# Kernel tuning notes

Measured on AMD Instinct MI355X. Metric: run time of the kernel, lower is better.

## Reference

```python
import jax, jax.numpy as jnp
import numpy as np

N_EMBD = 1024
N_HEAD = 16
HEAD_SIZE = N_EMBD // N_HEAD
SEQ_LEN = 2048


def setup_inputs() -> dict:
    key = jax.random.key(0)
    k_x, k_wa, k_ba, k_wp, k_bp = jax.random.split(key, 5)
    s = 0.02
    return {
        "x": jax.random.normal(k_x, (4, SEQ_LEN, N_EMBD), dtype=jnp.float32),
        "w_attn": jax.random.normal(k_wa, (N_EMBD, 3 * N_EMBD), dtype=jnp.float32) * s,
        "b_attn": jax.random.normal(k_ba, (3 * N_EMBD,), dtype=jnp.float32) * s,
        "w_proj": jax.random.normal(k_wp, (N_EMBD, N_EMBD), dtype=jnp.float32) * s,
        "b_proj": jax.random.normal(k_bp, (N_EMBD,), dtype=jnp.float32) * s,
    }


def reference(x, w_attn, b_attn, w_proj, b_proj):
    B, T, C = x.shape
    H, D = N_HEAD, HEAD_SIZE
    qkv = x @ w_attn + b_attn                      # [B,T,3C]
    q, k, v = jnp.split(qkv, 3, axis=-1)
    q = q.reshape(B, T, H, D).transpose(0, 2, 1, 3)  # [B,H,T,D]
    k = k.reshape(B, T, H, D).transpose(0, 2, 1, 3)
    v = v.reshape(B, T, H, D).transpose(0, 2, 1, 3)
    att = jnp.einsum('bhqd,bhkd->bhqk', q, k) / jnp.sqrt(jnp.float32(D))
    causal = jnp.tril(jnp.ones((T, T), dtype=bool))
    att = jnp.where(causal[None, None], att, jnp.float32(-jnp.inf))
    att = jax.nn.softmax(att, axis=-1)
    out = jnp.einsum('bhqk,bhkd->bhqd', att, v)    # [B,H,T,D]
    out = out.transpose(0, 2, 1, 3).reshape(B, T, C)
    return out @ w_proj + b_proj
```

## Files before the change

kernel.cpp:

```cpp
#include <hip/hip_runtime.h>

typedef short short8 __attribute__((ext_vector_type(8)));
typedef short short4v __attribute__((ext_vector_type(4)));
typedef float f32x4 __attribute__((ext_vector_type(4)));
typedef unsigned uint2v __attribute__((ext_vector_type(2)));

__device__ __forceinline__ float bf2f(short b) {
  unsigned u = ((unsigned)(unsigned short)b) << 16;
  return __builtin_bit_cast(float, u);
}
__device__ __forceinline__ short f2bf(float f) {
  unsigned u = __builtin_bit_cast(unsigned, f);
  u += 0x7fffu + ((u >> 16) & 1u);
  return (short)(u >> 16);
}
__device__ __forceinline__ unsigned cvt_pk_bf16(float lo, float hi) {
  unsigned r;
  asm("v_cvt_pk_bf16_f32 %0, %1, %2" : "=v"(r) : "v"(lo), "v"(hi));
  return r;
}

__device__ __forceinline__ void gload_lds16(const void* g, void* l) {
  __builtin_amdgcn_global_load_lds(
      (const __attribute__((address_space(1))) unsigned int*)g,
      (__attribute__((address_space(3))) unsigned int*)l, 16, 0, 0);
}

__device__ __forceinline__ short8 lds_frag(const short* tile, int row, int kc, int l4) {
  int chunk = (kc * 4 + l4) ^ (row & 7);
  return *(const short8*)&tile[row * 64 + chunk * 8];
}

__global__ __launch_bounds__(256) void k_convert_bf16(const float* __restrict__ in,
                                                      short* __restrict__ out, int n8) {
  int i = blockIdx.x * 256 + threadIdx.x;
  if (i >= n8) return;
  const float4* p = (const float4*)in;
  float4 a = p[2 * i], b = p[2 * i + 1];
  short8 o;
  o[0] = f2bf(a.x); o[1] = f2bf(a.y); o[2] = f2bf(a.z); o[3] = f2bf(a.w);
  o[4] = f2bf(b.x); o[5] = f2bf(b.y); o[6] = f2bf(b.z); o[7] = f2bf(b.w);
  ((short8*)out)[i] = o;
}

__global__ __launch_bounds__(256) void k_transpose_w(const float* __restrict__ w,
                                                     short* __restrict__ wT, int K, int N) {
  __shared__ float t[32][33];
  int nt = N >> 5;
  int rt = blockIdx.x / nt, ct = blockIdx.x % nt;
  int tx = threadIdx.x & 31, ty = threadIdx.x >> 5;
#pragma unroll
  for (int i = 0; i < 4; ++i) {
    int r = ty * 4 + i;
    t[r][tx] = w[(size_t)(rt * 32 + r) * N + ct * 32 + tx];
  }
  __syncthreads();
#pragma unroll
  for (int i = 0; i < 4; ++i) {
    int r = ty * 4 + i;
    wT[(size_t)(ct * 32 + r) * K + rt * 32 + tx] = f2bf(t[tx][r]);
  }
}

template <bool BF16OUT>
__global__ __launch_bounds__(512, 1) void k_gemm8p(const short* __restrict__ A,
                                                   const short* __restrict__ Bt,
                                                   const float* __restrict__ bias,
                                                   void* __restrict__ Cout,
                                                   int M, int N, int K) {
  __shared__ __align__(16) short Ab[2][256 * 64];
  __shared__ __align__(16) short Bb[2][256 * 64];
  int nt = N >> 8;
  int nwg = gridDim.x;
  int bid = blockIdx.x;
  int swz = (bid & 7) * (nwg >> 3) + (bid >> 3);
  int mt = swz / nt, ct = swz % nt;
  int tid = threadIdx.x, w = tid >> 6, lane = tid & 63;
  int l15 = lane & 15, l4 = lane >> 4;
  int wm = w >> 2, wn = w & 3;
  const short* Abase = A + (size_t)mt * 256 * K;
  const short* Bbase = Bt + (size_t)ct * 256 * K;
  int NT = K >> 6;

  int srow = lane >> 3;
  int slc = (lane & 7) ^ srow;

  auto stage = [&](const short* gbase, short* dstTile, int kt, int half) {
#pragma unroll
    for (int i = 0; i < 2; ++i) {
      int rowg = half * 128 + i * 64 + w * 8;
      gload_lds16(gbase + (size_t)(rowg + srow) * K + kt * 64 + slc * 8,
                  dstTile + (size_t)rowg * 64);
    }
  };

  f32x4 acc[8][4];
#pragma unroll
  for (int m = 0; m < 8; ++m)
#pragma unroll
    for (int n = 0; n < 4; ++n) acc[m][n] = f32x4{0.f, 0.f, 0.f, 0.f};

  stage(Bbase, &Bb[0][0], 0, 0);
  stage(Bbase, &Bb[0][0], 0, 1);
  stage(Abase, &Ab[0][0], 0, 0);
  stage(Abase, &Ab[0][0], 0, 1);
  stage(Bbase, &Bb[1][0], 1, 0);
  stage(Bbase, &Bb[1][0], 1, 1);
  stage(Abase, &Ab[1][0], 1, 0);
  stage(Abase, &Ab[1][0], 1, 1);
  asm volatile("s_waitcnt vmcnt(8)" ::: "memory");
  __builtin_amdgcn_s_barrier();

  for (int t = 0; t < NT; ++t) {
    int b = t & 1;
    const short* At = &Ab[b][0];
    const short* Btl = &Bb[b][0];
    short* Aw = &Ab[b][0];
    short* Bw = &Bb[b][0];
    bool pre = (t + 2 < NT);

    short8 aflo[4][2], bflo[2][2], bfhi[2][2], afhi[4][2];
#pragma unroll
    for (int mq = 0; mq < 4; ++mq)
#pragma unroll
      for (int kc = 0; kc < 2; ++kc)
        aflo[mq][kc] = lds_frag(At, wm * 128 + mq * 16 + l15, kc, l4);
#pragma unroll
    for (int nq = 0; nq < 2; ++nq)
#pragma unroll
      for (int kc = 0; kc < 2; ++kc)
        bflo[nq][kc] = lds_frag(Btl, wn * 64 + nq * 16 + l15, kc, l4);
    __builtin_amdgcn_s_barrier();
    asm volatile("s_waitcnt lgkmcnt(0)" ::: "memory");
    __builtin_amdgcn_sched_barrier(0);
    __builtin_amdgcn_s_setprio(1);
#pragma unroll
    for (int mq = 0; mq < 4; ++mq)
#pragma unroll
      for (int nq = 0; nq < 2; ++nq)
#pragma unroll
        for (int kc = 0; kc < 2; ++kc)
          acc[mq][nq] = __builtin_amdgcn_mfma_f32_16x16x32_bf16(aflo[mq][kc], bflo[nq][kc], acc[mq][nq], 0, 0, 0);
    __builtin_amdgcn_s_setprio(0);
    __builtin_amdgcn_s_barrier();

#pragma unroll
    for (int nq = 0; nq < 2; ++nq)
#pragma unroll
      for (int kc = 0; kc < 2; ++kc)
        bfhi[nq][kc] = lds_frag(Btl, wn * 64 + 32 + nq * 16 + l15, kc, l4);
    __builtin_amdgcn_s_barrier();
    asm volatile("s_waitcnt lgkmcnt(0)" ::: "memory");
    __builtin_amdgcn_sched_barrier(0);
    __builtin_amdgcn_s_setprio(1);
#pragma unroll
    for (int mq = 0; mq < 4; ++mq)
#pragma unroll
      for (int nq = 0; nq < 2; ++nq)
#pragma unroll
        for (int kc = 0; kc < 2; ++kc)
          acc[mq][2 + nq] = __builtin_amdgcn_mfma_f32_16x16x32_bf16(aflo[mq][kc], bfhi[nq][kc], acc[mq][2 + nq], 0, 0, 0);
    __builtin_amdgcn_s_setprio(0);
    __builtin_amdgcn_s_barrier();

#pragma unroll
    for (int mq = 0; mq < 4; ++mq)
#pragma unroll
      for (int kc = 0; kc < 2; ++kc)
        afhi[mq][kc] = lds_frag(At, wm * 128 + 64 + mq * 16 + l15, kc, l4);
    if (pre) {
      stage(Bbase, Bw, t + 2, 0);
      stage(Bbase, Bw, t + 2, 1);
    }
    __builtin_amdgcn_s_barrier();
    asm volatile("s_waitcnt lgkmcnt(0)" ::: "memory");
    __builtin_amdgcn_sched_barrier(0);
    __builtin_amdgcn_s_setprio(1);
#pragma unroll
    for (int mq = 0; mq < 4; ++mq)
#pragma unroll
      for (int nq = 0; nq < 2; ++nq)
#pragma unroll
        for (int kc = 0; kc < 2; ++kc)
          acc[4 + mq][2 + nq] = __builtin_amdgcn_mfma_f32_16x16x32_bf16(afhi[mq][kc], bfhi[nq][kc], acc[4 + mq][2 + nq], 0, 0, 0);
    __builtin_amdgcn_s_setprio(0);
    __builtin_amdgcn_s_barrier();

    if (pre) {
      stage(Abase, Aw, t + 2, 0);
      stage(Abase, Aw, t + 2, 1);
    }
    __builtin_amdgcn_s_setprio(1);
#pragma unroll
    for (int mq = 0; mq < 4; ++mq)
#pragma unroll
      for (int nq = 0; nq < 2; ++nq)
#pragma unroll
        for (int kc = 0; kc < 2; ++kc)
          acc[4 + mq][nq] = __builtin_amdgcn_mfma_f32_16x16x32_bf16(afhi[mq][kc], bflo[nq][kc], acc[4 + mq][nq], 0, 0, 0);
    __builtin_amdgcn_s_setprio(0);
    if (pre) {
      asm volatile("s_waitcnt vmcnt(8)" ::: "memory");
    } else if (t + 1 < NT) {
      asm volatile("s_waitcnt vmcnt(0)" ::: "memory");
    }
    __builtin_amdgcn_s_barrier();
  }

#pragma unroll
  for (int m = 0; m < 8; ++m) {
#pragma unroll
    for (int n = 0; n < 4; ++n) {
      int row = mt * 256 + wm * 128 + m * 16 + l4 * 4;
      int col = ct * 256 + wn * 64 + n * 16 + l15;
      float bv = bias[col];
#pragma unroll
      for (int j = 0; j < 4; ++j) {
        float v = acc[m][n][j] + bv;
        if constexpr (BF16OUT)
          ((short*)Cout)[(size_t)(row + j) * N + col] = f2bf(v);
        else
          ((float*)Cout)[(size_t)(row + j) * N + col] = v;
      }
    }
  }
}

template <bool BF16OUT>
__global__ __launch_bounds__(256) void k_gemm_bt(const short* __restrict__ A,
                                                 const short* __restrict__ Bt,
                                                 const float* __restrict__ bias,
                                                 void* __restrict__ Cout,
                                                 int M, int N, int K) {
  __shared__ __align__(16) short As[128 * 32];
  __shared__ __align__(16) short Bs[128 * 32];
  int nt = N >> 7;
  int mt = blockIdx.x / nt, ct = blockIdx.x % nt;
  int tid = threadIdx.x, w = tid >> 6, lane = tid & 63;
  int l15 = lane & 15, l4 = lane >> 4;
  int wr = (w >> 1) * 64, wc = (w & 1) * 64;
  const short* Abase = A + (size_t)mt * 128 * K;
  const short* Bbase = Bt + (size_t)ct * 128 * K;
  f32x4 acc[4][4];
#pragma unroll
  for (int m = 0; m < 4; ++m)
#pragma unroll
    for (int n = 0; n < 4; ++n) acc[m][n] = f32x4{0.f, 0.f, 0.f, 0.f};

  for (int kt = 0; kt < K; kt += 32) {
    __syncthreads();
#pragma unroll
    for (int i = 0; i < 2; ++i) {
      int idx = (w * 2 + i) * 64 + lane;
      gload_lds16(Abase + (size_t)(idx >> 2) * K + kt + (idx & 3) * 8, &As[(w * 2 + i) * 512]);
      gload_lds16(Bbase + (size_t)(idx >> 2) * K + kt + (idx & 3) * 8, &Bs[(w * 2 + i) * 512]);
    }
    __syncthreads();
    short8 af[4], bfr[4];
#pragma unroll
    for (int m = 0; m < 4; ++m) af[m] = *(const short8*)&As[(wr + m * 16 + l15) * 32 + l4 * 8];
#pragma unroll
    for (int n = 0; n < 4; ++n) bfr[n] = *(const short8*)&Bs[(wc + n * 16 + l15) * 32 + l4 * 8];
#pragma unroll
    for (int m = 0; m < 4; ++m)
#pragma unroll
      for (int n = 0; n < 4; ++n)
        acc[m][n] = __builtin_amdgcn_mfma_f32_16x16x32_bf16(af[m], bfr[n], acc[m][n], 0, 0, 0);
  }

#pragma unroll
  for (int m = 0; m < 4; ++m) {
#pragma unroll
    for (int n = 0; n < 4; ++n) {
      int row = mt * 128 + wr + m * 16 + l4 * 4;
      int col = ct * 128 + wc + n * 16 + l15;
      float bv = bias[col];
#pragma unroll
      for (int j = 0; j < 4; ++j) {
        float v = acc[m][n][j] + bv;
        if constexpr (BF16OUT)
          ((short*)Cout)[(size_t)(row + j) * N + col] = f2bf(v);
        else
          ((float*)Cout)[(size_t)(row + j) * N + col] = v;
      }
    }
  }
}

__global__ __launch_bounds__(256) void k_transpose_v(const short* __restrict__ qkv,
                                                     short* __restrict__ vT) {
  __shared__ __align__(16) short t[64][72];
  int blk = blockIdx.x;
  int tt = blk & 31, bh = blk >> 5;
  int batch = bh >> 4, h = bh & 15;
  int tid = threadIdx.x;
  const short* base = qkv + (size_t)(batch * 2048 + tt * 64) * 3072 + 2048 + h * 64;
#pragma unroll
  for (int rep = 0; rep < 2; ++rep) {
    int idx = rep * 256 + tid;
    int r = idx >> 3, dc = idx & 7;
    *(short8*)&t[r][dc * 8] = *(const short8*)(base + (size_t)r * 3072 + dc * 8);
  }
  __syncthreads();
  short* obase = vT + (size_t)bh * 64 * 2048 + tt * 64;
#pragma unroll
  for (int rep = 0; rep < 2; ++rep) {
    int idx = rep * 256 + tid;
    int d = idx >> 3, tc = idx & 7;
    short8 o;
#pragma unroll
    for (int i = 0; i < 8; ++i) o[i] = t[tc * 8 + i][d];
    *(short8*)(obase + (size_t)d * 2048 + tc * 8) = o;
  }
}

__global__ __launch_bounds__(256, 2) void k_attn(const short* __restrict__ qkv,
                                                 const short* __restrict__ vT,
                                                 short* __restrict__ out) {
  constexpr int T = 2048, C3 = 3072;
  __shared__ __align__(16) short Kl[2][64 * 72];
  __shared__ __align__(16) short P_lds[4][32 * 72];
  int bp = blockIdx.x & 7, bh = blockIdx.x >> 3;
  int batch = bh >> 4, h = bh & 15;
  int tid = threadIdx.x, w = tid >> 6, lane = tid & 63;
  int l15 = lane & 15, l4 = lane >> 4;

  int qt[2];
  qt[0] = 63 - (bp * 4 + w);
  qt[1] = bp * 4 + w;
  int lim[2] = {qt[0] >> 1, qt[1] >> 1};
  int ktb = (63 - bp * 4) >> 1;

  const short* kbase = qkv + (size_t)(batch * T) * C3 + 1024 + h * 64;
  const short* vbase = vT + (size_t)bh * 64 * T;

  int sr0 = tid >> 3, sr1 = 32 + (tid >> 3), sdc = (tid & 7) * 8;

  const float SCL = 0.18033688f;
  short8 qf[2][2][2];
#pragma unroll
  for (int t = 0; t < 2; ++t)
#pragma unroll
    for (int qc = 0; qc < 2; ++qc) {
      const short* qrow = qkv + (size_t)(batch * T + qt[t] * 32 + qc * 16 + l15) * C3 + h * 64;
#pragma unroll
      for (int kc = 0; kc < 2; ++kc) {
        short8 v = *(const short8*)(qrow + kc * 32 + l4 * 8);
#pragma unroll
        for (int i = 0; i < 8; ++i) v[i] = f2bf(bf2f(v[i]) * SCL);
        qf[t][qc][kc] = v;
      }
    }

  const f32x4 ZERO = f32x4{0.f, 0.f, 0.f, 0.f};
  short8 ONES;
#pragma unroll
  for (int i = 0; i < 8; ++i) ONES[i] = (short)0x3F80;

  f32x4 o_[2][2][4];
  f32x4 lacc[2][2];
#pragma unroll
  for (int t = 0; t < 2; ++t)
#pragma unroll
    for (int qc = 0; qc < 2; ++qc) {
      lacc[t][qc] = ZERO;
#pragma unroll
      for (int dt = 0; dt < 4; ++dt) o_[t][qc][dt] = ZERO;
    }

  {
    short8 a = *(const short8*)(kbase + (size_t)sr0 * C3 + sdc);
    short8 b = *(const short8*)(kbase + (size_t)sr1 * C3 + sdc);
    *(short8*)&Kl[0][sr0 * 72 + sdc] = a;
    *(short8*)&Kl[0][sr1 * 72 + sdc] = b;
  }
  __syncthreads();

  int cur = 0;
  for (int kt = 0; kt <= ktb; ++kt) {
    bool more = (kt < ktb);
    bool act0 = (kt <= lim[0]), act1 = (kt <= lim[1]);

    short8 pre0, pre1;
    if (more) {
      pre0 = *(const short8*)(kbase + (size_t)((kt + 1) * 64 + sr0) * C3 + sdc);
      pre1 = *(const short8*)(kbase + (size_t)((kt + 1) * 64 + sr1) * C3 + sdc);
    }

    const short* Kb = &Kl[cur][0];
    short8 kf[4][2];
#pragma unroll
    for (int kvt = 0; kvt < 4; ++kvt)
#pragma unroll
      for (int kc = 0; kc < 2; ++kc)
        kf[kvt][kc] = *(const short8*)(Kb + (kvt * 16 + l15) * 72 + kc * 32 + l4 * 8);

    short8 vf[4][2];
#pragma unroll
    for (int dt = 0; dt < 4; ++dt)
#pragma unroll
      for (int kc = 0; kc < 2; ++kc)
        vf[dt][kc] = *(const short8*)(vbase + (size_t)(dt * 16 + l15) * T + kt * 64 + kc * 32 + l4 * 8);

#pragma unroll
    for (int t = 0; t < 2; ++t) {
      bool act = (t == 0) ? act0 : act1;
      if (!act) continue;
      short* pb = &P_lds[w][0];

#pragma unroll
      for (int qc = 0; qc < 2; ++qc) {
        f32x4 s[4];
        __builtin_amdgcn_s_setprio(1);
#pragma unroll
        for (int kvt = 0; kvt < 4; ++kvt) {
          s[kvt] = __builtin_amdgcn_mfma_f32_16x16x32_bf16(kf[kvt][0], qf[t][qc][0], ZERO, 0, 0, 0);
          s[kvt] = __builtin_amdgcn_mfma_f32_16x16x32_bf16(kf[kvt][1], qf[t][qc][1], s[kvt], 0, 0, 0);
        }
        __builtin_amdgcn_s_setprio(0);

        if (kt == lim[t]) {
          int qg = qt[t] * 32 + qc * 16 + l15;
#pragma unroll
          for (int kvt = 0; kvt < 4; ++kvt)
#pragma unroll
            for (int j = 0; j < 4; ++j) {
              int kg = kt * 64 + kvt * 16 + l4 * 4 + j;
              if (kg > qg) s[kvt][j] = -1e30f;
            }
        }

#pragma unroll
        for (int kvt = 0; kvt < 4; ++kvt) {
          float p0 = exp2f(s[kvt][0]);
          float p1 = exp2f(s[kvt][1]);
          float p2 = exp2f(s[kvt][2]);
          float p3 = exp2f(s[kvt][3]);
          unsigned lo = cvt_pk_bf16(p0, p1);
          unsigned hi = cvt_pk_bf16(p2, p3);
          *(uint2v*)(pb + (qc * 16 + l15) * 72 + kvt * 16 + l4 * 4) = uint2v{lo, hi};
        }
      }

      asm volatile("s_waitcnt lgkmcnt(0)" ::: "memory");

      __builtin_amdgcn_s_setprio(1);
#pragma unroll
      for (int qc = 0; qc < 2; ++qc)
#pragma unroll
        for (int kc = 0; kc < 2; ++kc) {
          short8 pf = *(const short8*)(pb + (qc * 16 + l15) * 72 + kc * 32 + l4 * 8);
          lacc[t][qc] = __builtin_amdgcn_mfma_f32_16x16x32_bf16(ONES, pf, lacc[t][qc], 0, 0, 0);
#pragma unroll
          for (int dt = 0; dt < 4; ++dt)
            o_[t][qc][dt] = __builtin_amdgcn_mfma_f32_16x16x32_bf16(vf[dt][kc], pf, o_[t][qc][dt], 0, 0, 0);
        }
      __builtin_amdgcn_s_setprio(0);
    }

    if (more) {
      *(short8*)&Kl[cur ^ 1][sr0 * 72 + sdc] = pre0;
      *(short8*)&Kl[cur ^ 1][sr1 * 72 + sdc] = pre1;
    }
    __syncthreads();
    cur ^= 1;
  }

#pragma unroll
  for (int t = 0; t < 2; ++t) {
#pragma unroll
    for (int qc = 0; qc < 2; ++qc) {
      float inv = 1.f / lacc[t][qc][0];
      size_t rowb = (size_t)(batch * T + qt[t] * 32 + qc * 16 + l15) * 1024 + h * 64;
#pragma unroll
      for (int dt = 0; dt < 4; ++dt) {
        short4v pk4;
#pragma unroll
        for (int j = 0; j < 4; ++j) pk4[j] = f2bf(o_[t][qc][dt][j] * inv);
        *(short4v*)(out + rowb + dt * 16 + l4 * 4) = pk4;
      }
    }
  }
}

extern "C" void kernel_launch(void* const* d_in, const int* in_sizes, int n_in,
                              void* d_out, int out_size, void* d_ws, size_t ws_size,
                              hipStream_t stream) {
  const float* x      = (const float*)d_in[0];
  const float* w_attn = (const float*)d_in[1];
  const float* b_attn = (const float*)d_in[2];
  const float* w_proj = (const float*)d_in[3];
  const float* b_proj = (const float*)d_in[4];
  float* out = (float*)d_out;

  char* ws = (char*)d_ws;
  short* xb   = (short*)(ws);
  short* waT  = (short*)(ws + 16777216);
  short* wpT  = (short*)(ws + 23068672);
  short* qkv  = (short*)(ws + 25165824);
  short* vT   = (short*)(ws + 75497472);
  short* attn = xb;

  k_convert_bf16<<<4096, 256, 0, stream>>>(x, xb, 1048576);
  k_transpose_w<<<32 * 96, 256, 0, stream>>>(w_attn, waT, 1024, 3072);
  k_transpose_w<<<32 * 32, 256, 0, stream>>>(w_proj, wpT, 1024, 1024);
  k_gemm8p<true><<<384, 512, 0, stream>>>(xb, waT, b_attn, qkv, 8192, 3072, 1024);
  k_transpose_v<<<2048, 256, 0, stream>>>(qkv, vT);
  k_attn<<<512, 256, 0, stream>>>(qkv, vT, attn);
  k_gemm_bt<false><<<64 * 8, 256, 0, stream>>>(attn, wpT, b_proj, out, 8192, 1024, 1024);
}
```

Baseline: 198.7 us.

## Split attention KV loop across warps with LDS reduction, 4x more blocks

Each block now handles one pair of query tiles (one early, one late) instead of four warps each owning its own pair. The four warps split the KV tiles among themselves, striding by 4, and load K directly from global memory instead of staging it through double-buffered LDS. Partial O and row-sum accumulators are then reduced through LDS before normalisation. The goal is more blocks (2048) and higher occupancy (launch bounds 4), in exchange for uncoalesced direct K loads and an extra serialized cross-warp reduction with several barriers.

```diff
diff --git a/kernel.cpp b/kernel.cpp
--- a/kernel.cpp
+++ b/kernel.cpp
@@ -314,27 +314,23 @@
   }
 }
 
-__global__ __launch_bounds__(256, 2) void k_attn(const short* __restrict__ qkv,
+__global__ __launch_bounds__(256, 4) void k_attn(const short* __restrict__ qkv,
                                                  const short* __restrict__ vT,
                                                  short* __restrict__ out) {
   constexpr int T = 2048, C3 = 3072;
-  __shared__ __align__(16) short Kl[2][64 * 72];
   __shared__ __align__(16) short P_lds[4][32 * 72];
-  int bp = blockIdx.x & 7, bh = blockIdx.x >> 3;
+  int p = blockIdx.x & 31, bh = blockIdx.x >> 5;
   int batch = bh >> 4, h = bh & 15;
   int tid = threadIdx.x, w = tid >> 6, lane = tid & 63;
   int l15 = lane & 15, l4 = lane >> 4;
 
   int qt[2];
-  qt[0] = 63 - (bp * 4 + w);
-  qt[1] = bp * 4 + w;
+  qt[0] = 63 - p;
+  qt[1] = p;
   int lim[2] = {qt[0] >> 1, qt[1] >> 1};
-  int ktb = (63 - bp * 4) >> 1;
 
   const short* kbase = qkv + (size_t)(batch * T) * C3 + 1024 + h * 64;
   const short* vbase = vT + (size_t)bh * 64 * T;
-
-  int sr0 = tid >> 3, sr1 = 32 + (tid >> 3), sdc = (tid & 7) * 8;
 
   const float SCL = 0.18033688f;
   short8 qf[2][2][2];
@@ -368,32 +364,17 @@
       for (int dt = 0; dt < 4; ++dt) o_[t][qc][dt] = ZERO;
     }
 
-  {
-    short8 a = *(const short8*)(kbase + (size_t)sr0 * C3 + sdc);
-    short8 b = *(const short8*)(kbase + (size_t)sr1 * C3 + sdc);
-    *(short8*)&Kl[0][sr0 * 72 + sdc] = a;
-    *(short8*)&Kl[0][sr1 * 72 + sdc] = b;
-  }
-  __syncthreads();
-
-  int cur = 0;
-  for (int kt = 0; kt <= ktb; ++kt) {
-    bool more = (kt < ktb);
-    bool act0 = (kt <= lim[0]), act1 = (kt <= lim[1]);
-
-    short8 pre0, pre1;
-    if (more) {
-      pre0 = *(const short8*)(kbase + (size_t)((kt + 1) * 64 + sr0) * C3 + sdc);
-      pre1 = *(const short8*)(kbase + (size_t)((kt + 1) * 64 + sr1) * C3 + sdc);
-    }
-
-    const short* Kb = &Kl[cur][0];
+  short* pb = &P_lds[w][0];
+
+  for (int kt = w; kt <= lim[0]; kt += 4) {
+    bool act1 = (kt <= lim[1]);
+
     short8 kf[4][2];
 #pragma unroll
     for (int kvt = 0; kvt < 4; ++kvt)
 #pragma unroll
       for (int kc = 0; kc < 2; ++kc)
-        kf[kvt][kc] = *(const short8*)(Kb + (kvt * 16 + l15) * 72 + kc * 32 + l4 * 8);
+        kf[kvt][kc] = *(const short8*)(kbase + (size_t)(kt * 64 + kvt * 16 + l15) * C3 + kc * 32 + l4 * 8);
 
     short8 vf[4][2];
 #pragma unroll
@@ -404,9 +385,7 @@
 
 #pragma unroll
     for (int t = 0; t < 2; ++t) {
-      bool act = (t == 0) ? act0 : act1;
-      if (!act) continue;
-      short* pb = &P_lds[w][0];
+      if (t == 1 && !act1) continue;
 
 #pragma unroll
       for (int qc = 0; qc < 2; ++qc) {
@@ -457,29 +436,45 @@
         }
       __builtin_amdgcn_s_setprio(0);
     }
-
-    if (more) {
-      *(short8*)&Kl[cur ^ 1][sr0 * 72 + sdc] = pre0;
-      *(short8*)&Kl[cur ^ 1][sr1 * 72 + sdc] = pre1;
-    }
+  }
+
+  __syncthreads();
+  float* ob = (float*)&P_lds[0][0];
+  float* lb = ob + 4096;
+#pragma unroll
+  for (int s = 0; s < 4; ++s) {
+    int t = s >> 1, qc = s & 1;
+#pragma unroll
+    for (int dt = 0; dt < 4; ++dt)
+      *(f32x4*)(ob + ((size_t)(w * 64 + lane)) * 16 + dt * 4) = o_[t][qc][dt];
+    lb[w * 64 + lane] = lacc[t][qc][0];
     __syncthreads();
-    cur ^= 1;
-  }
-
-#pragma unroll
-  for (int t = 0; t < 2; ++t) {
-#pragma unroll
-    for (int qc = 0; qc < 2; ++qc) {
-      float inv = 1.f / lacc[t][qc][0];
+    if (w == s) {
+      f32x4 osum0 = *(f32x4*)(ob + (size_t)lane * 16);
+      f32x4 osum1 = *(f32x4*)(ob + (size_t)lane * 16 + 4);
+      f32x4 osum2 = *(f32x4*)(ob + (size_t)lane * 16 + 8);
+      f32x4 osum3 = *(f32x4*)(ob + (size_t)lane * 16 + 12);
+      float lsum = lb[lane];
+#pragma unroll
+      for (int ww = 1; ww < 4; ++ww) {
+        osum0 += *(f32x4*)(ob + ((size_t)(ww * 64 + lane)) * 16);
+        osum1 += *(f32x4*)(ob + ((size_t)(ww * 64 + lane)) * 16 + 4);
+        osum2 += *(f32x4*)(ob + ((size_t)(ww * 64 + lane)) * 16 + 8);
+        osum3 += *(f32x4*)(ob + ((size_t)(ww * 64 + lane)) * 16 + 12);
+        lsum += lb[ww * 64 + lane];
+      }
+      float inv = 1.f / lsum;
       size_t rowb = (size_t)(batch * T + qt[t] * 32 + qc * 16 + l15) * 1024 + h * 64;
+      f32x4 os[4] = {osum0, osum1, osum2, osum3};
 #pragma unroll
       for (int dt = 0; dt < 4; ++dt) {
         short4v pk4;
 #pragma unroll
-        for (int j = 0; j < 4; ++j) pk4[j] = f2bf(o_[t][qc][dt][j] * inv);
+        for (int j = 0; j < 4; ++j) pk4[j] = f2bf(os[dt][j] * inv);
         *(short4v*)(out + rowb + dt * 16 + l4 * 4) = pk4;
       }
     }
+    __syncthreads();
   }
 }
 
@@ -506,6 +501,6 @@
   k_transpose_w<<<32 * 32, 256, 0, stream>>>(w_proj, wpT, 1024, 1024);
   k_gemm8p<true><<<384, 512, 0, stream>>>(xb, waT, b_attn, qkv, 8192, 3072, 1024);
   k_transpose_v<<<2048, 256, 0, stream>>>(qkv, vT);
-  k_attn<<<512, 256, 0, stream>>>(qkv, vT, attn);
+  k_attn<<<2048, 256, 0, stream>>>(qkv, vT, attn);
   k_gemm_bt<false><<<64 * 8, 256, 0, stream>>>(attn, wpT, b_proj, out, 8192, 1024, 1024);
 }
```

Result: slower. 463.8 us (+133.4%).

## Fuse V transpose into QKV GEMM epilogue and remap attention blocks per XCD

Applied to the files above, without the earlier changes.

The QKV GEMM epilogue now writes the V columns directly in transposed [B,H,D,T] layout as packed 4-element stores. This removes the separate k_transpose_v kernel launch and its extra read/write of V. The attention kernel's block index mapping is also changed so that blocks sharing a head land on the same XCD, which should improve L2 reuse of K/V. In exchange, the GEMM epilogue does strided 8-byte stores for the V columns, which are less coalesced than the normal row-major stores.

```diff
diff --git a/kernel.cpp b/kernel.cpp
--- a/kernel.cpp
+++ b/kernel.cpp
@@ -67,6 +67,7 @@
                                                    const short* __restrict__ Bt,
                                                    const float* __restrict__ bias,
                                                    void* __restrict__ Cout,
+                                                   short* __restrict__ vTout,
                                                    int M, int N, int K) {
   __shared__ __align__(16) short Ab[2][256 * 64];
   __shared__ __align__(16) short Bb[2][256 * 64];
@@ -214,13 +215,23 @@
       int row = mt * 256 + wm * 128 + m * 16 + l4 * 4;
       int col = ct * 256 + wn * 64 + n * 16 + l15;
       float bv = bias[col];
-#pragma unroll
-      for (int j = 0; j < 4; ++j) {
-        float v = acc[m][n][j] + bv;
-        if constexpr (BF16OUT)
-          ((short*)Cout)[(size_t)(row + j) * N + col] = f2bf(v);
-        else
-          ((float*)Cout)[(size_t)(row + j) * N + col] = v;
+      if constexpr (BF16OUT) {
+        short4v pk4;
+#pragma unroll
+        for (int j = 0; j < 4; ++j) pk4[j] = f2bf(acc[m][n][j] + bv);
+        if (col >= 2048) {
+          int hh = (col - 2048) >> 6, dd = (col - 2048) & 63;
+          int batch2 = row >> 11, tok = row & 2047;
+          *(short4v*)(vTout + (((size_t)(batch2 * 16 + hh) * 64 + dd) << 11) + tok) = pk4;
+        } else {
+#pragma unroll
+          for (int j = 0; j < 4; ++j)
+            ((short*)Cout)[(size_t)(row + j) * N + col] = pk4[j];
+        }
+      } else {
+#pragma unroll
+        for (int j = 0; j < 4; ++j)
+          ((float*)Cout)[(size_t)(row + j) * N + col] = acc[m][n][j] + bv;
       }
     }
   }
@@ -287,40 +298,15 @@
   }
 }
 
-__global__ __launch_bounds__(256) void k_transpose_v(const short* __restrict__ qkv,
-                                                     short* __restrict__ vT) {
-  __shared__ __align__(16) short t[64][72];
-  int blk = blockIdx.x;
-  int tt = blk & 31, bh = blk >> 5;
-  int batch = bh >> 4, h = bh & 15;
-  int tid = threadIdx.x;
-  const short* base = qkv + (size_t)(batch * 2048 + tt * 64) * 3072 + 2048 + h * 64;
-#pragma unroll
-  for (int rep = 0; rep < 2; ++rep) {
-    int idx = rep * 256 + tid;
-    int r = idx >> 3, dc = idx & 7;
-    *(short8*)&t[r][dc * 8] = *(const short8*)(base + (size_t)r * 3072 + dc * 8);
-  }
-  __syncthreads();
-  short* obase = vT + (size_t)bh * 64 * 2048 + tt * 64;
-#pragma unroll
-  for (int rep = 0; rep < 2; ++rep) {
-    int idx = rep * 256 + tid;
-    int d = idx >> 3, tc = idx & 7;
-    short8 o;
-#pragma unroll
-    for (int i = 0; i < 8; ++i) o[i] = t[tc * 8 + i][d];
-    *(short8*)(obase + (size_t)d * 2048 + tc * 8) = o;
-  }
-}
-
 __global__ __launch_bounds__(256, 2) void k_attn(const short* __restrict__ qkv,
                                                  const short* __restrict__ vT,
                                                  short* __restrict__ out) {
   constexpr int T = 2048, C3 = 3072;
   __shared__ __align__(16) short Kl[2][64 * 72];
   __shared__ __align__(16) short P_lds[4][32 * 72];
-  int bp = blockIdx.x & 7, bh = blockIdx.x >> 3;
+  int i_ = blockIdx.x;
+  int xcd = i_ & 7, m_ = i_ >> 3;
+  int bh = xcd * 8 + (m_ & 7), bp = m_ >> 3;
   int batch = bh >> 4, h = bh & 15;
   int tid = threadIdx.x, w = tid >> 6, lane = tid & 63;
   int l15 = lane & 15, l4 = lane >> 4;
@@ -504,8 +490,7 @@
   k_convert_bf16<<<4096, 256, 0, stream>>>(x, xb, 1048576);
   k_transpose_w<<<32 * 96, 256, 0, stream>>>(w_attn, waT, 1024, 3072);
   k_transpose_w<<<32 * 32, 256, 0, stream>>>(w_proj, wpT, 1024, 1024);
-  k_gemm8p<true><<<384, 512, 0, stream>>>(xb, waT, b_attn, qkv, 8192, 3072, 1024);
-  k_transpose_v<<<2048, 256, 0, stream>>>(qkv, vT);
+  k_gemm8p<true><<<384, 512, 0, stream>>>(xb, waT, b_attn, qkv, vT, 8192, 3072, 1024);
   k_attn<<<512, 256, 0, stream>>>(qkv, vT, attn);
   k_gemm_bt<false><<<64 * 8, 256, 0, stream>>>(attn, wpT, b_proj, out, 8192, 1024, 1024);
 }
```

Result: no change. 198.4 us (-0.2%).
